# Performance work log

Hardware: AMD Instinct MI355X
Metric: run time of the kernel (lower is better)

The kernel has to match this reference:

```python
import jax, jax.numpy as jnp
import numpy as np

B, T, D, HEADS, HW = 4, 64, 512, 8, 14
DH = D // HEADS
N = HW * HW
GAMMA, BIAS_ADJ, ALPHA, MASK_RATE = 0.6, 0.2, 0.2, 0.7
CIN_FM = 768
CLS_HIDDEN = 512
K = int(MASK_RATE * T)


def distance_adj(bsz, t):
    # DistanceAdj: adj[i,j] = exp(-|gamma*(i-j)^2 + bias|), shared across batch
    i = jnp.arange(t, dtype=jnp.float32)
    d2 = (i[:, None] - i[None, :]) ** 2
    adj = jnp.exp(-jnp.abs(GAMMA * d2 + BIAS_ADJ))
    return jnp.broadcast_to(adj[None], (bsz, t, t))


def topk_mask_adj(x, adj):
    # x: [Bn,T,C]; keep adj rows AND cols at top-k feature-magnitude indices
    mag = jnp.linalg.norm(x, axis=2)                    # [Bn,T]
    idx = jax.lax.top_k(mag, K)[1]                      # [Bn,K]
    bn = x.shape[0]
    sel = jnp.zeros((bn, x.shape[1]), bool).at[jnp.arange(bn)[:, None], idx].set(True)
    mask = sel[:, :, None] | sel[:, None, :]            # row OR col selected
    return jnp.where(mask, adj, 0.0)


def gat_multihead(x, adj, W, a1, a2):
    # x [Bn,T,C]; W [H,C,Dh]; a1,a2 [H,Dh]. concat=True -> ELU on concat output.
    h = jnp.einsum('btc,hcd->bhtd', x, W)
    e = jnp.einsum('bhtd,hd->bht', h, a1)[:, :, :, None] + \
        jnp.einsum('bhtd,hd->bht', h, a2)[:, :, None, :]
    e = jax.nn.leaky_relu(e, ALPHA)
    e = jnp.where(adj[:, None, :, :] > 0, e, -9e15)
    attn = jax.nn.softmax(e, axis=-1)
    out = jnp.einsum('bhij,bhjd->bhid', attn, h)
    bn, hds, t, dh = out.shape
    out = out.transpose(0, 2, 1, 3).reshape(bn, t, hds * dh)
    return jax.nn.elu(out)


def layernorm(x, g, b, eps=1e-5):
    m = x.mean(-1, keepdims=True)
    v = ((x - m) ** 2).mean(-1, keepdims=True)
    return (x - m) / jnp.sqrt(v + eps) * g + b


def signed_sqrt(x):
    # == sqrt(relu(x)) - sqrt(relu(-x))
    return jnp.sign(x) * jnp.sqrt(jnp.abs(x))


def temporal_block(x, W, a1, a2, lin_w, lin_b, ln_g, ln_b):
    # shared body of TemporalModule / FeatureMapTemporalModule (eval mode)
    adj = distance_adj(x.shape[0], x.shape[1])
    adj = topk_mask_adj(x, adj)
    tmp = gat_multihead(x, adj, W, a1, a2)
    tmp = signed_sqrt(tmp)
    # F.normalize default dim=1 (over T), clamp_min eps
    tmp = tmp / jnp.maximum(jnp.linalg.norm(tmp, axis=1, keepdims=True), 1e-12)
    x = x + tmp @ lin_w.T + lin_b
    return layernorm(x, ln_g, ln_b)


def _forward(x_v, feature_map, pre_w, pre_b, post_w, post_b,
             tm_W, tm_a1, tm_a2, tm_lin_w, tm_lin_b, tm_ln_g, tm_ln_b,
             fm_W, fm_a1, fm_a2, fm_lin_w, fm_lin_b, fm_ln_g, fm_ln_b,
             cls_w1, cls_b1, cls_w2, cls_b2):
    # pre head: 1x1 Conv2d 768->512 + ReLU (Dropout2d off in eval)
    fm = jnp.einsum('nchw,oc->nohw', feature_map, pre_w) + pre_b[None, :, None, None]
    fm = jax.nn.relu(fm)
    ano = fm.reshape(B, T, D, HW, HW)

    # TemporalModule on pooled features -> [B,512,T]
    xv = temporal_block(x_v, tm_W, tm_a1, tm_a2, tm_lin_w, tm_lin_b, tm_ln_g, tm_ln_b)
    xv = xv.transpose(0, 2, 1)

    # FeatureMapTemporalModule: [B,T,512,14,14] -> [B*N,T,512] graphs
    a = ano.reshape(B, T, D, N).transpose(0, 3, 1, 2).reshape(B * N, T, D)
    a = temporal_block(a, fm_W, fm_a1, fm_a2, fm_lin_w, fm_lin_b, fm_ln_g, fm_ln_b)
    # permute(0,2,1) -> [BN,D,T]; view(B,N,D,T).permute(0,3,2,1) -> [B,T,D,N]
    a = a.transpose(0, 2, 1).reshape(B, N, D, T).transpose(0, 3, 2, 1)
    a = a.reshape(B, T, D, HW, HW)

    # post head: 1x1 Conv2d 512->1
    pm = jnp.einsum('btchw,oc->btohw', a, post_w) + post_b[None, None, :, None, None]
    ano_map = pm.reshape(B, T, 1, HW, HW)

    # classifier: Conv1d(512->cls)->GELU->Conv1d(cls->1) on [B,512,T]
    h = jnp.einsum('bct,oc->bot', xv, cls_w1) + cls_b1[None, :, None]
    h = jax.nn.gelu(h, approximate=False)
    logits = jnp.einsum('bct,oc->bot', h, cls_w2) + cls_b2[None, :, None]
    logits = logits.transpose(0, 2, 1)                  # [B,T,1]
    return logits, ano_map


def setup_inputs():
    key = jax.random.key(0)
    ks = jax.random.split(key, 16)
    rn = lambda i, shape, s=0.02: jax.random.normal(ks[i], shape, jnp.float32) * s
    z = lambda *s: jnp.zeros(s, jnp.float32)
    return {
        'x_v': jax.random.normal(ks[0], (B, T, D), jnp.float32),
        'feature_map': jax.random.normal(ks[1], (B * T, CIN_FM, HW, HW), jnp.float32),
        'pre_w': rn(2, (D, CIN_FM)), 'pre_b': z(D),
        'post_w': rn(3, (1, D)), 'post_b': z(1),
        'tm_W': rn(4, (HEADS, D, DH)), 'tm_a1': rn(5, (HEADS, DH)), 'tm_a2': rn(6, (HEADS, DH)),
        'tm_lin_w': rn(7, (D, D)), 'tm_lin_b': z(D),
        'tm_ln_g': jnp.ones((D,), jnp.float32), 'tm_ln_b': z(D),
        'fm_W': rn(8, (HEADS, D, DH)), 'fm_a1': rn(9, (HEADS, DH)), 'fm_a2': rn(10, (HEADS, DH)),
        'fm_lin_w': rn(11, (D, D)), 'fm_lin_b': z(D),
        'fm_ln_g': jnp.ones((D,), jnp.float32), 'fm_ln_b': z(D),
        'cls_w1': rn(12, (CLS_HIDDEN, D)), 'cls_b1': z(CLS_HIDDEN),
        'cls_w2': rn(13, (1, CLS_HIDDEN)), 'cls_b2': z(1),
    }


def reference(x_v, feature_map, pre_w, pre_b, post_w, post_b,
              tm_W, tm_a1, tm_a2, tm_lin_w, tm_lin_b, tm_ln_g, tm_ln_b,
              fm_W, fm_a1, fm_a2, fm_lin_w, fm_lin_b, fm_ln_g, fm_ln_b,
              cls_w1, cls_b1, cls_w2, cls_b2):
    return _forward(x_v, feature_map, pre_w, pre_b, post_w, post_b,
                    tm_W, tm_a1, tm_a2, tm_lin_w, tm_lin_b, tm_ln_g, tm_ln_b,
                    fm_W, fm_a1, fm_a2, fm_lin_w, fm_lin_b, fm_ln_g, fm_ln_b,
                    cls_w1, cls_b1, cls_w2, cls_b2)
```

## Files before the change

kernel.cpp:

```cpp
#include <hip/hip_runtime.h>
#include <cstdint>
#include <cstddef>

constexpr int TT   = 64;
constexpr int DD   = 512;
constexpr int NHEAD= 8;
constexpr int DHH  = 64;
constexpr int NPIX = 196;
constexpr int CIN  = 768;
constexpr int KSEL = 44;
constexpr int NG_FM= 784;
constexpr int NIMG = 256;
constexpr int DBAND = 12;

typedef __attribute__((ext_vector_type(8))) short bf16x8;
typedef __attribute__((ext_vector_type(4))) float f32x4;

__device__ __forceinline__ short bfr(float x) {
  union { float f; unsigned u; } v; v.f = x;
  unsigned r = (v.u + 0x7fffu + ((v.u >> 16) & 1u)) >> 16;
  return (short)r;
}
__device__ __forceinline__ float bf2f(short s) {
  return __uint_as_float(((unsigned)(unsigned short)s) << 16);
}

__global__ void k_prepPW2(const float* __restrict__ pw, short* __restrict__ hi,
                          short* __restrict__ lo)
{
  int m = blockIdx.x * 256 + threadIdx.x;
  int o = m / 96, kc = m - o * 96;
  int mt = o >> 6, ot = (o >> 4) & 3, lr = o & 15;
  int ks = kc >> 2, lg = kc & 3;
  size_t addr = ((((size_t)(mt * 4 + ot) * 24 + ks) * 64 + lg * 16 + lr)) * 8;
  const float* src = pw + (size_t)o * CIN + kc * 8;
  #pragma unroll
  for (int j = 0; j < 8; j++) {
    float x = src[j];
    unsigned u = __float_as_uint(x);
    hi[addr + j] = (short)(u >> 16);
    lo[addr + j] = bfr(x - __uint_as_float(u & 0xffff0000u));
  }
}

__global__ __launch_bounds__(256) void k_prepFM3(
    const float* __restrict__ fmap, short* __restrict__ fh,
    short* __restrict__ fl, int n0)
{
  __shared__ float ar[64][197];
  const int cc = blockIdx.x;
  const int nl = blockIdx.y;
  const int tid = threadIdx.x;
  const float* src = fmap + ((size_t)(n0 + nl) * CIN + cc * 64) * NPIX;
  for (int i = tid; i < 64 * 49; i += 256) {
    int c = i / 49, q = i - c * 49;
    float4 v = *(const float4*)&src[(size_t)c * NPIX + q * 4];
    *(float4*)&ar[c][q * 4] = v;
  }
  __syncthreads();
  for (int i = tid; i < 208 * 8; i += 256) {
    int hw = i >> 3, kc = i & 7;
    int ks = cc * 2 + (kc >> 2), lg = kc & 3;
    size_t addr = ((((size_t)nl * 13 + (hw >> 4)) * 24 + ks) * 64 + lg * 16 + (hw & 15)) * 8;
    union { short s[8]; bf16x8 v; } hh, ll;
    #pragma unroll
    for (int j = 0; j < 8; j++) {
      float x = (hw < NPIX) ? ar[kc * 8 + j][hw] : 0.f;
      unsigned u = __float_as_uint(x);
      hh.s[j] = (short)(u >> 16);
      ll.s[j] = bfr(x - __uint_as_float(u & 0xffff0000u));
    }
    *(bf16x8*)&fh[addr] = hh.v;
    *(bf16x8*)&fl[addr] = ll.v;
  }
}

__global__ __launch_bounds__(256) void k_preconv3(
    const short* __restrict__ fmfh, const short* __restrict__ fmfl,
    const short* __restrict__ pwfh, const short* __restrict__ pwfl,
    const float* __restrict__ pb, short* __restrict__ axb,
    double* __restrict__ sums, int n0)
{
  __shared__ float arena[7616];
  const int wg = blockIdx.x;
  const int mt = (wg >> 3) & 7;
  const int nl = (wg & 7) | ((wg >> 6) << 3);
  const int n  = n0 + nl;
  const int b  = n >> 6, t = n & 63;
  const int tid = threadIdx.x;
  const int w = tid >> 6, l = tid & 63;
  const int lr = l & 15, lg = l >> 4;
  const int o0 = mt * 64;

  const int hwt0 = (w == 0) ? 0 : 1 + 3 * w;
  const int nq   = (w == 0) ? 4 : 3;

  f32x4 acc[4][4];
  #pragma unroll
  for (int q = 0; q < 4; q++)
    #pragma unroll
    for (int ot = 0; ot < 4; ot++) acc[q][ot] = (f32x4){0.f, 0.f, 0.f, 0.f};

  for (int ks = 0; ks < 24; ks++) {
    bf16x8 Ah[4], Al[4];
    #pragma unroll
    for (int ot = 0; ot < 4; ot++) {
      size_t off = (((size_t)(mt * 4 + ot) * 24 + ks) * 64 + l) * 8;
      Ah[ot] = *(const bf16x8*)&pwfh[off];
      Al[ot] = *(const bf16x8*)&pwfl[off];
    }
    #pragma unroll
    for (int q = 0; q < 4; q++) if (q < nq) {
      size_t boff = ((((size_t)nl * 13 + hwt0 + q) * 24 + ks) * 64 + l) * 8;
      bf16x8 Bh = *(const bf16x8*)&fmfh[boff];
      bf16x8 Bl = *(const bf16x8*)&fmfl[boff];
      #pragma unroll
      for (int ot = 0; ot < 4; ot++) {
        acc[q][ot] = __builtin_amdgcn_mfma_f32_16x16x32_bf16(Al[ot], Bh, acc[q][ot], 0, 0, 0);
        acc[q][ot] = __builtin_amdgcn_mfma_f32_16x16x32_bf16(Ah[ot], Bl, acc[q][ot], 0, 0, 0);
        acc[q][ot] = __builtin_amdgcn_mfma_f32_16x16x32_bf16(Ah[ot], Bh, acc[q][ot], 0, 0, 0);
      }
    }
  }

  float4 pbf[4];
  #pragma unroll
  for (int ot = 0; ot < 4; ot++)
    pbf[ot] = *(const float4*)&pb[o0 + ot * 16 + 4 * lg];

  #pragma unroll
  for (int pass = 0; pass < 2; pass++) {
    const int tbase = pass ? 7 : 0;
    const int tend  = pass ? 13 : 7;
    const int rbase = tbase * 16;
    const int rows  = (tend - tbase) * 16;
    __syncthreads();
    #pragma unroll
    for (int q = 0; q < 4; q++) if (q < nq) {
      int hwt = hwt0 + q;
      if (hwt >= tbase && hwt < tend) {
        int row_l = hwt * 16 + lr - rbase;
        #pragma unroll
        for (int ot = 0; ot < 4; ot++) {
          int col = (ot * 16 + 4 * lg + 4 * row_l) % 68;
          f32x4 a = acc[q][ot];
          float4 o4v;
          o4v.x = fmaxf(a[0] + pbf[ot].x, 0.f);
          o4v.y = fmaxf(a[1] + pbf[ot].y, 0.f);
          o4v.z = fmaxf(a[2] + pbf[ot].z, 0.f);
          o4v.w = fmaxf(a[3] + pbf[ot].w, 0.f);
          *(float4*)&arena[row_l * 68 + col] = o4v;
        }
      }
    }
    __syncthreads();
    for (int i = tid; i < rows * 16; i += 256) {
      int row_l = i >> 4, o4 = i & 15;
      int hw = rbase + row_l;
      float4 v = make_float4(0.f, 0.f, 0.f, 0.f);
      if (hw < NPIX) {
        int col = (o4 * 4 + 4 * row_l) % 68;
        v = *(const float4*)&arena[row_l * 68 + col];
        size_t idx = ((size_t)(b * NPIX + hw) * TT + t) * DD + o0 + o4 * 4;
        *(short4*)&axb[idx] = make_short4(bfr(v.x), bfr(v.y), bfr(v.z), bfr(v.w));
      }
      double vs = (double)v.x * v.x + (double)v.y * v.y
                + (double)v.z * v.z + (double)v.w * v.w;
      vs += __shfl_xor(vs, 1); vs += __shfl_xor(vs, 2);
      vs += __shfl_xor(vs, 4); vs += __shfl_xor(vs, 8);
      if ((i & 15) == 0 && hw < NPIX)
        atomicAdd(&sums[(size_t)(b * NPIX + hw) * TT + t], vs);
    }
  }
}

__global__ void k_prepWb2(const float* __restrict__ W, short* __restrict__ o)
{
  int m = blockIdx.x * 256 + threadIdx.x;
  int j = m >> 6, kc = m & 63;
  int ks = kc >> 2, lg = kc & 3;
  size_t addr = (((size_t)(j >> 4) * 16 + ks) * 64 + lg * 16 + (j & 15)) * 8;
  #pragma unroll
  for (int jj = 0; jj < 8; jj++) {
    int k = kc * 8 + jj;
    o[addr + jj] = bfr(W[(size_t)(j >> 6) * (DD * DHH) + (size_t)k * DHH + (j & 63)]);
  }
}

__global__ void k_prepLWb2(const float* __restrict__ a, short* __restrict__ o)
{
  int m = blockIdx.x * 256 + threadIdx.x;
  int j = m >> 6, kc = m & 63;
  int ks = kc >> 2, lg = kc & 3;
  size_t addr = (((size_t)(j >> 4) * 16 + ks) * 64 + lg * 16 + (j & 15)) * 8;
  const float* src = a + (size_t)j * DD + kc * 8;
  #pragma unroll
  for (int jj = 0; jj < 8; jj++) o[addr + jj] = bfr(src[jj]);
}

__global__ void k_cvt(const float* __restrict__ a, short* __restrict__ o)
{
  int m = blockIdx.x * 256 + threadIdx.x;
  o[m] = bfr(a[m]);
}

__global__ void k_prepGP(const float* __restrict__ g, const float* __restrict__ b,
                         const float* __restrict__ pw, const float* __restrict__ pb,
                         float* __restrict__ gp, float* __restrict__ cst)
{
  __shared__ float red[256], red2[256];
  int tid = threadIdx.x;
  float s1 = 0.f, s2 = 0.f;
  for (int c = tid; c < 512; c += 256) {
    float gpv = g[c] * pw[c];
    gp[c] = gpv;
    s1 += gpv;
    s2 += b[c] * pw[c];
  }
  red[tid] = s1; red2[tid] = s2;
  __syncthreads();
  for (int s = 128; s > 0; s >>= 1) {
    if (tid < s) { red[tid] += red[tid + s]; red2[tid] += red2[tid + s]; }
    __syncthreads();
  }
  if (tid == 0) { cst[0] = red[0]; cst[1] = red2[0] + pb[0]; }
}

__global__ void k_topk(const float* __restrict__ x, unsigned long long* __restrict__ sel)
{
  int g = blockIdx.x, lane = threadIdx.x;
  const float* row = x + ((size_t)g * TT + lane) * DD;
  double s = 0.0;
  for (int dd = 0; dd < DD; dd += 4) {
    float4 v = *(const float4*)(row + dd);
    s += (double)v.x * (double)v.x + (double)v.y * (double)v.y
       + (double)v.z * (double)v.z + (double)v.w * (double)v.w;
  }
  __shared__ double mag[64];
  mag[lane] = s;
  __syncthreads();
  int rank = 0;
  for (int j = 0; j < 64; j++) {
    double m = mag[j];
    rank += (m > s) || (m == s && j < lane);
  }
  unsigned long long bal = __ballot(rank < KSEL);
  if (lane == 0) sel[g] = bal;
}

__global__ void k_topk2(const double* __restrict__ sums, unsigned long long* __restrict__ sel)
{
  int g = blockIdx.x, lane = threadIdx.x;
  double s = sums[(size_t)g * TT + lane];
  __shared__ double mag[64];
  mag[lane] = s;
  __syncthreads();
  int rank = 0;
  for (int j = 0; j < 64; j++) {
    double m = mag[j];
    rank += (m > s) || (m == s && j < lane);
  }
  unsigned long long bal = __ballot(rank < KSEL);
  if (lane == 0) sel[g] = bal;
}

__global__ __launch_bounds__(256) void k_gemm(
    const short* __restrict__ Ab, const short* __restrict__ Bbf,
    const float* __restrict__ bias, const float* __restrict__ Res,
    float* __restrict__ Outf, short* __restrict__ Outb,
    int Mtiles, int swz)
{
  __shared__ short Asl[2][128 * 40];
  const int wg = blockIdx.x;
  int mt, nt;
  if (swz) { int xcd = wg & 7, idx = wg >> 3; mt = xcd * (Mtiles >> 3) + (idx >> 2); nt = idx & 3; }
  else     { mt = wg >> 2; nt = wg & 3; }
  const int m0 = mt * 128, n0 = nt * 128;
  const int tid = threadIdx.x;
  const int l  = tid & 63;
  const int lr = l & 15, lg = l >> 4;
  const int wm = (tid >> 7) & 1, wn = (tid >> 6) & 1;

  const int srow = tid >> 1, skq = tid & 1;
  const short* gA = Ab + (size_t)(m0 + srow) * DD + skq * 16;
  const int soff = srow * 40 + skq * 16;

  bf16x8 ra0 = *(const bf16x8*)(gA);
  bf16x8 ra1 = *(const bf16x8*)(gA + 8);
  *(bf16x8*)&Asl[0][soff]     = ra0;
  *(bf16x8*)&Asl[0][soff + 8] = ra1;
  __syncthreads();

  f32x4 acc[4][4] = {};
  for (int ks = 0; ks < 16; ks++) {
    const int cur = ks & 1;
    if (ks < 15) {
      const int k0 = (ks + 1) * 32;
      ra0 = *(const bf16x8*)(gA + k0);
      ra1 = *(const bf16x8*)(gA + k0 + 8);
    }
    bf16x8 af[4], bfv[4];
    #pragma unroll
    for (int mi = 0; mi < 4; mi++)
      af[mi] = *(const bf16x8*)&Asl[cur][(wm * 64 + mi * 16 + lr) * 40 + lg * 8];
    #pragma unroll
    for (int ni = 0; ni < 4; ni++) {
      size_t boff = (((size_t)(nt * 8 + wn * 4 + ni) * 16 + ks) * 64 + l) * 8;
      bfv[ni] = *(const bf16x8*)&Bbf[boff];
    }
    #pragma unroll
    for (int mi = 0; mi < 4; mi++)
      #pragma unroll
      for (int ni = 0; ni < 4; ni++)
        acc[mi][ni] = __builtin_amdgcn_mfma_f32_16x16x32_bf16(af[mi], bfv[ni], acc[mi][ni], 0, 0, 0);
    if (ks < 15) {
      *(bf16x8*)&Asl[cur ^ 1][soff]     = ra0;
      *(bf16x8*)&Asl[cur ^ 1][soff + 8] = ra1;
      __syncthreads();
    }
  }

  #pragma unroll
  for (int mi = 0; mi < 4; mi++) {
    #pragma unroll
    for (int r = 0; r < 4; r++) {
      const size_t row = (size_t)(m0 + wm * 64 + mi * 16 + lg * 4 + r);
      #pragma unroll
      for (int ni = 0; ni < 4; ni++) {
        const int col = n0 + wn * 64 + ni * 16 + lr;
        float v = acc[mi][ni][r];
        if (bias) v += bias[col];
        if (Res)  v += Res[row * DD + col];
        if (Outf) Outf[row * DD + col] = v;
        if (Outb) Outb[row * DD + col] = bfr(v);
      }
    }
  }
}

__global__ __launch_bounds__(256) void k_gemm2ln(
    const short* __restrict__ Ab, const short* __restrict__ Bbf,
    const float* __restrict__ bias, const short* __restrict__ Resb,
    const float* __restrict__ gp, const float* __restrict__ cst,
    float* __restrict__ outp)
{
  __shared__ short Asl[32 * 520];
  __shared__ float red[2][32][3];
  const int wg = blockIdx.x;
  const int xcd = wg & 7, idx = wg >> 3;
  const int g = xcd * 98 + (idx >> 1);
  const int half = idx & 1;
  const int m0 = g * 64 + half * 32;
  const int tid = threadIdx.x;
  const int w = tid >> 6, l = tid & 63;
  const int lr = l & 15, lg = l >> 4;
  const int rowb = (w & 1) * 16;
  const int ch  = w >> 1;
  const int ntb = ch * 16;

  #pragma unroll
  for (int i = 0; i < 8; i++) {
    int c = tid + i * 256;
    int row = c >> 6, off = (c & 63) * 8;
    *(bf16x8*)&Asl[row * 520 + off] =
        *(const bf16x8*)&Ab[(size_t)(m0 + row) * DD + off];
  }
  __syncthreads();

  f32x4 acc[16];
  #pragma unroll
  for (int i = 0; i < 16; i++) acc[i] = (f32x4){0.f, 0.f, 0.f, 0.f};

  for (int ks = 0; ks < 16; ks++) {
    bf16x8 af = *(const bf16x8*)&Asl[(rowb + lr) * 520 + ks * 32 + lg * 8];
    #pragma unroll
    for (int ntl = 0; ntl < 16; ntl++) {
      bf16x8 bb = *(const bf16x8*)&Bbf[(((size_t)(ntb + ntl) * 16 + ks) * 64 + l) * 8];
      acc[ntl] = __builtin_amdgcn_mfma_f32_16x16x32_bf16(af, bb, acc[ntl], 0, 0, 0);
    }
  }

  float sum[4] = {0.f,0.f,0.f,0.f}, sumsq[4] = {0.f,0.f,0.f,0.f}, dgp[4] = {0.f,0.f,0.f,0.f};
  #pragma unroll
  for (int ntl = 0; ntl < 16; ntl++) {
    int col = (ntb + ntl) * 16 + lr;
    float bi  = bias[col];
    float gpv = gp[col];
    #pragma unroll
    for (int r = 0; r < 4; r++) {
      size_t row = (size_t)(m0 + rowb + lg * 4 + r);
      float v = acc[ntl][r] + bi + bf2f(Resb[row * DD + col]);
      sum[r] += v; sumsq[r] += v * v; dgp[r] += v * gpv;
    }
  }
  #pragma unroll
  for (int r = 0; r < 4; r++) {
    #pragma unroll
    for (int mof = 1; mof <= 8; mof <<= 1) {
      sum[r]   += __shfl_xor(sum[r], mof);
      sumsq[r] += __shfl_xor(sumsq[r], mof);
      dgp[r]   += __shfl_xor(dgp[r], mof);
    }
    if (lr == 0) {
      int rl = rowb + lg * 4 + r;
      red[ch][rl][0] = sum[r]; red[ch][rl][1] = sumsq[r]; red[ch][rl][2] = dgp[r];
    }
  }
  __syncthreads();
  if (tid < 32) {
    float S = red[0][tid][0] + red[1][tid][0];
    float Q = red[0][tid][1] + red[1][tid][1];
    float D = red[0][tid][2] + red[1][tid][2];
    float mean = S * (1.f / 512.f);
    float var  = Q * (1.f / 512.f) - mean * mean;
    float rstd = rsqrtf(var + 1e-5f);
    const int b = g / NPIX, hw = g - b * NPIX;
    const int t = half * 32 + tid;
    outp[(size_t)b * (TT * NPIX) + t * NPIX + hw] = rstd * (D - mean * cst[0]) + cst[1];
  }
}

__global__ __launch_bounds__(256) void k_attn(
    short* __restrict__ tmp, const float* __restrict__ a1v,
    const float* __restrict__ a2v, const unsigned long long* __restrict__ sel)
{
  __shared__ float hs[64][68];
  __shared__ float attnv[64][68];
  __shared__ float s1[64], s2[64], aw[128], cnorm[64];
  const int h = blockIdx.x, g = blockIdx.y;
  const int tid = threadIdx.x;
  const int r = tid >> 4, c = tid & 15;
  short* base = tmp + (size_t)g * TT * DD + h * DHH;

  for (int i = tid; i < 4096; i += 256) {
    int t = i >> 6, dh = i & 63;
    hs[t][dh] = bf2f(base[(size_t)t * DD + dh]);
  }
  if (tid < 128) aw[tid] = (tid < 64) ? a1v[h * 64 + tid] : a2v[h * 64 + (tid - 64)];
  __syncthreads();

  const int i4 = tid >> 2, sub = tid & 3;
  {
    float v1 = 0.f, v2 = 0.f;
    #pragma unroll
    for (int q = 0; q < 16; q++) {
      int dh = sub * 16 + q;
      float hv = hs[i4][dh];
      v1 += hv * aw[dh]; v2 += hv * aw[64 + dh];
    }
    v1 += __shfl_xor(v1, 1); v1 += __shfl_xor(v1, 2);
    v2 += __shfl_xor(v2, 1); v2 += __shfl_xor(v2, 2);
    if (sub == 0) { s1[i4] = v1; s2[i4] = v2; }
  }
  __syncthreads();

  const unsigned long long sm = sel[g];
  {
    const bool seli = (sm >> i4) & 1ULL;
    const float vi = s1[i4];
    float ev[16];
    float mx = -1e30f;
    #pragma unroll
    for (int q = 0; q < 16; q++) {
      int j = sub * 16 + q;
      float e = vi + s2[j];
      e = e >= 0.f ? e : 0.2f * e;
      int dist = i4 > j ? i4 - j : j - i4;
      bool ok = (seli || ((sm >> j) & 1ULL)) && (dist <= DBAND);
      e = ok ? e : -9e15f;
      ev[q] = e;
      mx = fmaxf(mx, e);
    }
    mx = fmaxf(mx, __shfl_xor(mx, 1));
    mx = fmaxf(mx, __shfl_xor(mx, 2));
    float sum = 0.f;
    #pragma unroll
    for (int q = 0; q < 16; q++) { ev[q] = expf(ev[q] - mx); sum += ev[q]; }
    sum += __shfl_xor(sum, 1); sum += __shfl_xor(sum, 2);
    float inv = 1.f / sum;
    #pragma unroll
    for (int q = 0; q < 16; q++) attnv[i4][sub * 16 + q] = ev[q] * inv;
  }
  __syncthreads();

  float oc[4][4];
  #pragma unroll
  for (int i = 0; i < 4; i++)
    #pragma unroll
    for (int j = 0; j < 4; j++) oc[i][j] = 0.f;
  for (int j = 0; j < 64; j++) {
    float p[4];
    #pragma unroll
    for (int di = 0; di < 4; di++) p[di] = attnv[r * 4 + di][j];
    float4 hv = *(const float4*)&hs[j][c * 4];
    float hb[4] = {hv.x, hv.y, hv.z, hv.w};
    #pragma unroll
    for (int di = 0; di < 4; di++)
      #pragma unroll
      for (int dj = 0; dj < 4; dj++)
        oc[di][dj] += p[di] * hb[dj];
  }

  float cs4[4] = {0.f, 0.f, 0.f, 0.f};
  #pragma unroll
  for (int di = 0; di < 4; di++)
    #pragma unroll
    for (int dj = 0; dj < 4; dj++) {
      float v = oc[di][dj];
      v = v > 0.f ? v : expm1f(v);
      v = v >= 0.f ? sqrtf(v) : -sqrtf(-v);
      oc[di][dj] = v;
      cs4[dj] += v * v;
    }
  __syncthreads();
  *(float4*)&attnv[r][c * 4] = make_float4(cs4[0], cs4[1], cs4[2], cs4[3]);
  __syncthreads();
  if (tid < 64) {
    float ssum = 0.f;
    for (int rr = 0; rr < 16; rr++) ssum += attnv[rr][tid];
    cnorm[tid] = fmaxf(sqrtf(ssum), 1e-12f);
  }
  __syncthreads();
  float4 cn = *(const float4*)&cnorm[c * 4];
  float inv4[4] = {1.f / cn.x, 1.f / cn.y, 1.f / cn.z, 1.f / cn.w};
  #pragma unroll
  for (int di = 0; di < 4; di++) {
    short4 s4 = make_short4(bfr(oc[di][0] * inv4[0]), bfr(oc[di][1] * inv4[1]),
                            bfr(oc[di][2] * inv4[2]), bfr(oc[di][3] * inv4[3]));
    *(short4*)&base[(size_t)(r * 4 + di) * DD + c * 4] = s4;
  }
}

__global__ void k_ln(float* __restrict__ x, const float* __restrict__ gam, const float* __restrict__ bet)
{
  const size_t row = blockIdx.x;
  const int lane = threadIdx.x;
  float* p = x + row * DD + lane * 8;
  float4 v0 = *(float4*)p;
  float4 v1 = *(float4*)(p + 4);
  float va[8] = {v0.x, v0.y, v0.z, v0.w, v1.x, v1.y, v1.z, v1.w};
  float s = 0.f;
  #pragma unroll
  for (int i = 0; i < 8; i++) s += va[i];
  #pragma unroll
  for (int m = 32; m >= 1; m >>= 1) s += __shfl_xor(s, m);
  float mean = s * (1.f / 512.f);
  float q = 0.f;
  #pragma unroll
  for (int i = 0; i < 8; i++) { float d = va[i] - mean; q += d * d; }
  #pragma unroll
  for (int m = 32; m >= 1; m >>= 1) q += __shfl_xor(q, m);
  float rstd = rsqrtf(q * (1.f / 512.f) + 1e-5f);
  const float* gp = gam + lane * 8;
  const float* bp = bet + lane * 8;
  float4 g0 = *(const float4*)gp, g1 = *(const float4*)(gp + 4);
  float4 b0 = *(const float4*)bp, b1 = *(const float4*)(bp + 4);
  float ga[8] = {g0.x, g0.y, g0.z, g0.w, g1.x, g1.y, g1.z, g1.w};
  float ba[8] = {b0.x, b0.y, b0.z, b0.w, b1.x, b1.y, b1.z, b1.w};
  float o[8];
  #pragma unroll
  for (int i = 0; i < 8; i++) o[i] = (va[i] - mean) * rstd * ga[i] + ba[i];
  *(float4*)p       = make_float4(o[0], o[1], o[2], o[3]);
  *(float4*)(p + 4) = make_float4(o[4], o[5], o[6], o[7]);
}

__global__ __launch_bounds__(256) void k_cls(
    const float* __restrict__ xv, const float* __restrict__ w1,
    const float* __restrict__ b1, const float* __restrict__ w2,
    const float* __restrict__ b2, float* __restrict__ outp)
{
  const int m = blockIdx.x;
  const int tid = threadIdx.x;
  __shared__ float xr[512];
  __shared__ float red[256];
  xr[tid] = xv[(size_t)m * DD + tid];
  xr[tid + 256] = xv[(size_t)m * DD + tid + 256];
  __syncthreads();
  float part = 0.f;
  for (int o = tid; o < 512; o += 256) {
    const float* wr = w1 + (size_t)o * DD;
    float d = 0.f;
    for (int cc = 0; cc < DD; cc += 4) {
      float4 wv = *(const float4*)(wr + cc);
      d += wv.x * xr[cc] + wv.y * xr[cc + 1] + wv.z * xr[cc + 2] + wv.w * xr[cc + 3];
    }
    d += b1[o];
    float ge = 0.5f * d * (1.0f + erff(d * 0.70710678118654752f));
    part += ge * w2[o];
  }
  red[tid] = part;
  __syncthreads();
  for (int s = 128; s > 0; s >>= 1) {
    if (tid < s) red[tid] += red[tid + s];
    __syncthreads();
  }
  if (tid == 0) outp[m] = red[0] + b2[0];
}

extern "C" void kernel_launch(void* const* d_in, const int* in_sizes, int n_in,
                              void* d_out, int out_size, void* d_ws, size_t ws_size,
                              hipStream_t stream)
{
  const float* x_v    = (const float*)d_in[0];
  const float* fmap   = (const float*)d_in[1];
  const float* pre_w  = (const float*)d_in[2];
  const float* pre_b  = (const float*)d_in[3];
  const float* post_w = (const float*)d_in[4];
  const float* post_b = (const float*)d_in[5];
  const float* tm_W   = (const float*)d_in[6];
  const float* tm_a1  = (const float*)d_in[7];
  const float* tm_a2  = (const float*)d_in[8];
  const float* tm_lw  = (const float*)d_in[9];
  const float* tm_lb  = (const float*)d_in[10];
  const float* tm_g   = (const float*)d_in[11];
  const float* tm_b   = (const float*)d_in[12];
  const float* fm_W   = (const float*)d_in[13];
  const float* fm_a1  = (const float*)d_in[14];
  const float* fm_a2  = (const float*)d_in[15];
  const float* fm_lw  = (const float*)d_in[16];
  const float* fm_lb  = (const float*)d_in[17];
  const float* fm_g   = (const float*)d_in[18];
  const float* fm_b   = (const float*)d_in[19];
  const float* c_w1   = (const float*)d_in[20];
  const float* c_b1   = (const float*)d_in[21];
  const float* c_w2   = (const float*)d_in[22];
  const float* c_b2   = (const float*)d_in[23];
  float* out = (float*)d_out;

  short* axb    = (short*)d_ws;
  short* tmpb   = axb + 25690112;
  float* xtm    = (float*)(tmpb + 25690112);
  short* xvb    = (short*)(xtm + 131072);
  short* tmptmb = xvb + 131072;
  short* WTb_fm = tmptmb + 131072;
  short* WTb_tm = WTb_fm + 262144;
  short* LWb_fm = WTb_tm + 262144;
  short* LWb_tm = LWb_fm + 262144;
  short* pwf_hi = LWb_tm + 262144;
  short* pwf_lo = pwf_hi + 393216;
  unsigned long long* sel_fm = (unsigned long long*)(pwf_lo + 393216);
  unsigned long long* sel_tm = sel_fm + 784;
  double* sums  = (double*)(sel_tm + 4);
  float* gp     = (float*)(sums + 50176);
  float* cst    = gp + 512;
  short* fmh = (short*)(cst + 2);
  short* fml = fmh + 20447232;

  hipMemsetAsync(sums, 0, (size_t)NG_FM * TT * sizeof(double), stream);

  k_prepPW2<<<192, 256, 0, stream>>>(pre_w, pwf_hi, pwf_lo);
  k_prepWb2<<<128, 256, 0, stream>>>(fm_W, WTb_fm);
  k_prepWb2<<<128, 256, 0, stream>>>(tm_W, WTb_tm);
  k_prepLWb2<<<128, 256, 0, stream>>>(fm_lw, LWb_fm);
  k_prepLWb2<<<128, 256, 0, stream>>>(tm_lw, LWb_tm);
  k_cvt<<<512, 256, 0, stream>>>(x_v, xvb);
  k_prepGP<<<1, 256, 0, stream>>>(fm_g, fm_b, post_w, post_b, gp, cst);

  for (int half = 0; half < 2; half++) {
    k_prepFM3<<<dim3(12, 128), 256, 0, stream>>>(fmap, fmh, fml, half * 128);
    k_preconv3<<<1024, 256, 0, stream>>>(fmh, fml, pwf_hi, pwf_lo, pre_b, axb, sums, half * 128);
  }

  k_topk2<<<NG_FM, 64, 0, stream>>>(sums, sel_fm);
  k_topk<<<4, 64, 0, stream>>>(x_v, sel_tm);

  k_gemm<<<1568, 256, 0, stream>>>(axb, WTb_fm, nullptr, nullptr, nullptr, tmpb, 392, 1);
  k_gemm<<<8, 256, 0, stream>>>(xvb, WTb_tm, nullptr, nullptr, nullptr, tmptmb, 2, 0);

  k_attn<<<dim3(NHEAD, NG_FM), 256, 0, stream>>>(tmpb, fm_a1, fm_a2, sel_fm);
  k_attn<<<dim3(NHEAD, 4), 256, 0, stream>>>(tmptmb, tm_a1, tm_a2, sel_tm);

  k_gemm2ln<<<1568, 256, 0, stream>>>(tmpb, LWb_fm, fm_lb, axb, gp, cst, out + 256);
  k_gemm<<<8, 256, 0, stream>>>(tmptmb, LWb_tm, tm_lb, x_v, xtm, nullptr, 2, 0);

  k_ln<<<NIMG, 64, 0, stream>>>(xtm, tm_g, tm_b);

  k_cls<<<NIMG, 256, 0, stream>>>(xtm, c_w1, c_b1, c_w2, c_b2, out);
}
```

Measured before the change: 647.5 us.

## Use bf16 MFMA for attention-weighted sum in GAT attention kernel

Replaces the scalar fp32 attn@h product in k_attn with bf16 MFMA 16x16x32 instructions. h is now staged in shared memory as bf16 in an MFMA-ready swizzled layout, and the a1/a2 score dot products are computed during that load. Output is written through LDS with 16-byte vector stores. Attention probabilities are now rounded to bf16 before the matmul, which slightly lowers precision. The kernel is likely a small fraction of total time.

```diff
diff --git a/kernel.cpp b/kernel.cpp
--- a/kernel.cpp
+++ b/kernel.cpp
@@ -424,38 +424,45 @@
     short* __restrict__ tmp, const float* __restrict__ a1v,
     const float* __restrict__ a2v, const unsigned long long* __restrict__ sel)
 {
-  __shared__ float hs[64][68];
-  __shared__ float attnv[64][68];
+  __shared__ short hb[4096];
+  __shared__ short attnb[64 * 72];
   __shared__ float s1[64], s2[64], aw[128], cnorm[64];
+  __shared__ float redc[4][4][16];
   const int h = blockIdx.x, g = blockIdx.y;
   const int tid = threadIdx.x;
-  const int r = tid >> 4, c = tid & 15;
+  const int w = tid >> 6, l = tid & 63;
+  const int lr = l & 15, lg = l >> 4;
   short* base = tmp + (size_t)g * TT * DD + h * DHH;
 
-  for (int i = tid; i < 4096; i += 256) {
-    int t = i >> 6, dh = i & 63;
-    hs[t][dh] = bf2f(base[(size_t)t * DD + dh]);
-  }
   if (tid < 128) aw[tid] = (tid < 64) ? a1v[h * 64 + tid] : a2v[h * 64 + (tid - 64)];
   __syncthreads();
 
-  const int i4 = tid >> 2, sub = tid & 3;
-  {
+  #pragma unroll
+  for (int p = 0; p < 2; p++) {
+    int c = tid + p * 256;
+    int t = c >> 3, k8 = c & 7;
+    bf16x8 v = *(const bf16x8*)&base[(size_t)t * DD + k8 * 8];
+    const int ct = k8 >> 1;
+    const int ks = t >> 5, lgk = (t >> 3) & 3, jj = t & 7;
+    const int cbase = ((ct * 2 + ks) * 64 + lgk * 16 + (k8 & 1) * 8) * 8 + jj;
     float v1 = 0.f, v2 = 0.f;
     #pragma unroll
-    for (int q = 0; q < 16; q++) {
-      int dh = sub * 16 + q;
-      float hv = hs[i4][dh];
-      v1 += hv * aw[dh]; v2 += hv * aw[64 + dh];
-    }
-    v1 += __shfl_xor(v1, 1); v1 += __shfl_xor(v1, 2);
-    v2 += __shfl_xor(v2, 1); v2 += __shfl_xor(v2, 2);
-    if (sub == 0) { s1[i4] = v1; s2[i4] = v2; }
+    for (int j = 0; j < 8; j++) {
+      float x = bf2f(v[j]);
+      int dh = k8 * 8 + j;
+      v1 += x * aw[dh];
+      v2 += x * aw[64 + dh];
+      hb[cbase + j * 8] = v[j];
+    }
+    v1 += __shfl_xor(v1, 1); v1 += __shfl_xor(v1, 2); v1 += __shfl_xor(v1, 4);
+    v2 += __shfl_xor(v2, 1); v2 += __shfl_xor(v2, 2); v2 += __shfl_xor(v2, 4);
+    if (k8 == 0) { s1[t] = v1; s2[t] = v2; }
   }
   __syncthreads();
 
   const unsigned long long sm = sel[g];
   {
+    const int i4 = tid >> 2, sub = tid & 3;
     const bool seli = (sm >> i4) & 1ULL;
     const float vi = s1[i4];
     float ev[16];
@@ -479,55 +486,63 @@
     sum += __shfl_xor(sum, 1); sum += __shfl_xor(sum, 2);
     float inv = 1.f / sum;
     #pragma unroll
-    for (int q = 0; q < 16; q++) attnv[i4][sub * 16 + q] = ev[q] * inv;
-  }
-  __syncthreads();
-
-  float oc[4][4];
-  #pragma unroll
-  for (int i = 0; i < 4; i++)
-    #pragma unroll
-    for (int j = 0; j < 4; j++) oc[i][j] = 0.f;
-  for (int j = 0; j < 64; j++) {
-    float p[4];
-    #pragma unroll
-    for (int di = 0; di < 4; di++) p[di] = attnv[r * 4 + di][j];
-    float4 hv = *(const float4*)&hs[j][c * 4];
-    float hb[4] = {hv.x, hv.y, hv.z, hv.w};
-    #pragma unroll
-    for (int di = 0; di < 4; di++)
-      #pragma unroll
-      for (int dj = 0; dj < 4; dj++)
-        oc[di][dj] += p[di] * hb[dj];
-  }
-
-  float cs4[4] = {0.f, 0.f, 0.f, 0.f};
-  #pragma unroll
-  for (int di = 0; di < 4; di++)
-    #pragma unroll
-    for (int dj = 0; dj < 4; dj++) {
-      float v = oc[di][dj];
+    for (int q = 0; q < 16; q++)
+      attnb[i4 * 72 + sub * 16 + q] = bfr(ev[q] * inv);
+  }
+  __syncthreads();
+
+  f32x4 acc[4];
+  #pragma unroll
+  for (int ct = 0; ct < 4; ct++) acc[ct] = (f32x4){0.f, 0.f, 0.f, 0.f};
+  #pragma unroll
+  for (int ks = 0; ks < 2; ks++) {
+    bf16x8 af = *(const bf16x8*)&attnb[(w * 16 + lr) * 72 + ks * 32 + lg * 8];
+    #pragma unroll
+    for (int ct = 0; ct < 4; ct++) {
+      bf16x8 bb = *(const bf16x8*)&hb[((ct * 2 + ks) * 64 + l) * 8];
+      acc[ct] = __builtin_amdgcn_mfma_f32_16x16x32_bf16(af, bb, acc[ct], 0, 0, 0);
+    }
+  }
+
+  float vv[4][4];
+  float cs[4] = {0.f, 0.f, 0.f, 0.f};
+  #pragma unroll
+  for (int ct = 0; ct < 4; ct++)
+    #pragma unroll
+    for (int r = 0; r < 4; r++) {
+      float v = acc[ct][r];
       v = v > 0.f ? v : expm1f(v);
       v = v >= 0.f ? sqrtf(v) : -sqrtf(-v);
-      oc[di][dj] = v;
-      cs4[dj] += v * v;
-    }
-  __syncthreads();
-  *(float4*)&attnv[r][c * 4] = make_float4(cs4[0], cs4[1], cs4[2], cs4[3]);
+      vv[ct][r] = v;
+      cs[ct] += v * v;
+    }
+  #pragma unroll
+  for (int ct = 0; ct < 4; ct++) {
+    cs[ct] += __shfl_xor(cs[ct], 16);
+    cs[ct] += __shfl_xor(cs[ct], 32);
+    if (lg == 0) redc[w][ct][lr] = cs[ct];
+  }
   __syncthreads();
   if (tid < 64) {
-    float ssum = 0.f;
-    for (int rr = 0; rr < 16; rr++) ssum += attnv[rr][tid];
-    cnorm[tid] = fmaxf(sqrtf(ssum), 1e-12f);
-  }
-  __syncthreads();
-  float4 cn = *(const float4*)&cnorm[c * 4];
-  float inv4[4] = {1.f / cn.x, 1.f / cn.y, 1.f / cn.z, 1.f / cn.w};
-  #pragma unroll
-  for (int di = 0; di < 4; di++) {
-    short4 s4 = make_short4(bfr(oc[di][0] * inv4[0]), bfr(oc[di][1] * inv4[1]),
-                            bfr(oc[di][2] * inv4[2]), bfr(oc[di][3] * inv4[3]));
-    *(short4*)&base[(size_t)(r * 4 + di) * DD + c * 4] = s4;
+    int ct = tid >> 4, c = tid & 15;
+    float S = redc[0][ct][c] + redc[1][ct][c] + redc[2][ct][c] + redc[3][ct][c];
+    cnorm[ct * 16 + c] = fmaxf(sqrtf(S), 1e-12f);
+  }
+  __syncthreads();
+  #pragma unroll
+  for (int ct = 0; ct < 4; ct++) {
+    float inv = 1.f / cnorm[ct * 16 + lr];
+    #pragma unroll
+    for (int r = 0; r < 4; r++)
+      attnb[(w * 16 + lg * 4 + r) * 72 + ct * 16 + lr] = bfr(vv[ct][r] * inv);
+  }
+  __syncthreads();
+  #pragma unroll
+  for (int p = 0; p < 2; p++) {
+    int c = tid + p * 256;
+    int t = c >> 3, k8 = c & 7;
+    *(bf16x8*)&base[(size_t)t * DD + k8 * 8] =
+        *(const bf16x8*)&attnb[t * 72 + k8 * 8];
   }
 }
 
```

New measurement: 610.2 us. 1.06x faster.
